# Performance work log

Measured on AMD Instinct MI355X. Metric: run time of the kernel, lower is better.

## Reference

```python
import jax, jax.numpy as jnp
import numpy as np

N = 50000      # num nodes
E = 800000     # num edges (before self loops)
H = 2          # heads
C = 64         # out_channels (== in_dim, extra_layer=False)
L = 3          # n_layer
SLOPE = 0.2    # leaky_relu negative_slope


def setup_inputs() -> dict:
    key = jax.random.key(0)
    k1, k2, k3 = jax.random.split(key, 3)
    x = jax.random.normal(k1, (N, C), dtype=jnp.float32)
    edge_index = jax.random.randint(k2, (2, E), 0, N)
    att = jax.random.normal(k3, (L, H, C), dtype=jnp.float32) * 0.1  # glorot-ish scale
    bias = jnp.zeros((L, C), dtype=jnp.float32)
    return {"x": x, "edge_index": edge_index, "att": att, "bias": bias}


def _segment_softmax(alpha, dst, n):
    # alpha: [Etot, H], softmax over edges sharing the same destination node
    m = jax.ops.segment_max(alpha, dst, num_segments=n)          # [N, H]
    a = jnp.exp(alpha - m[dst])                                  # [Etot, H]
    s = jax.ops.segment_sum(a, dst, num_segments=n)              # [N, H]
    return a / (s[dst] + 1e-16)


def _gat_layer(x, src, dst, att_l, bias_l):
    # extra_layer=False: x_l == x_r == x broadcast over heads, so x_i + x_j is
    # head-independent; compute it once as [Etot, C].
    m = jax.nn.leaky_relu(x[dst] + x[src], negative_slope=SLOPE)  # [Etot, C]
    alpha = m @ att_l.T                                           # [Etot, H]
    alpha = _segment_softmax(alpha, dst, N)
    # message = x_j * alpha, scatter-add to destinations, then mean over heads
    outs = [jax.ops.segment_sum(x[src] * alpha[:, h:h + 1], dst, num_segments=N)
            for h in range(H)]                                    # H x [N, C]
    return jnp.stack(outs, 0).mean(0) + bias_l                    # [N, C]


def reference(x, edge_index, att, bias):
    # add self loops (add_self_loops=True)
    loops = jnp.arange(N, dtype=edge_index.dtype)
    src = jnp.concatenate([edge_index[0], loops])
    dst = jnp.concatenate([edge_index[1], loops])
    feats = [x]
    h = x
    for l in range(L):
        h = _gat_layer(h, src, dst, att[l], bias[l])
        feats.append(h)
    return jnp.stack(feats, axis=1).mean(axis=1)  # [N, C]
```

## Files before the change

### kernel.cpp

```cpp
#include <hip/hip_runtime.h>
#include <hip/hip_bf16.h>

#define NN 50000
#define EE 800000
#define CC 64
#define HH 2
#define LL 3
#define CAP 64
#define NB 782
#define BCAP 1280
#define CHUNK 8192
#define NBLK ((EE + CHUNK - 1) / CHUNK)


__global__ __launch_bounds__(1024) void k_bin(const int* __restrict__ ei,
                                              int* __restrict__ bcnt,
                                              unsigned int* __restrict__ bucket) {
    __shared__ unsigned int stash[CHUNK];
    __shared__ int hist[NB];
    __shared__ int rank[NB];
    __shared__ int base[NB];

    int c0 = blockIdx.x * CHUNK;
    int n = EE - c0; if (n > CHUNK) n = CHUNK;

    for (int b = threadIdx.x; b < NB; b += 1024) { hist[b] = 0; rank[b] = 0; }
    __syncthreads();

    for (int k = threadIdx.x; k < n; k += 1024) {
        unsigned int s = (unsigned int)ei[c0 + k];
        unsigned int d = (unsigned int)ei[EE + c0 + k];
        stash[k] = (d << 16) | s;
        atomicAdd(&hist[d >> 6], 1);
    }
    __syncthreads();

    for (int b = threadIdx.x; b < NB; b += 1024) {
        int c = hist[b];
        base[b] = c ? atomicAdd(&bcnt[b], c) : 0;
    }
    __syncthreads();

    for (int k = threadIdx.x; k < n; k += 1024) {
        unsigned int pk = stash[k];
        int b = (int)(pk >> 22);
        int r = atomicAdd(&rank[b], 1);
        int pos = base[b] + r;
        if (pos < BCAP) bucket[(size_t)b * BCAP + pos] = pk;
    }
}

__global__ __launch_bounds__(256) void k_place(const unsigned int* __restrict__ bucket,
                                               const int* __restrict__ bcnt,
                                               int* __restrict__ cnt,
                                               unsigned short* __restrict__ slots) {
    __shared__ int lcnt[64];
    int b = blockIdx.x;
    if (threadIdx.x < 64) lcnt[threadIdx.x] = 0;
    __syncthreads();
    int node0 = b << 6;
    int m = bcnt[b];
    if (m > BCAP) m = BCAP;
    const unsigned int* src = bucket + (size_t)b * BCAP;
    for (int i = threadIdx.x; i < m; i += 256) {
        unsigned int pk = src[i];
        int d = (int)(pk >> 16);
        int s = (int)(pk & 0xFFFFu);
        int pos = atomicAdd(&lcnt[d - node0], 1);
        if (pos < CAP) slots[(size_t)d * CAP + pos] = (unsigned short)s;
    }
    __syncthreads();
    if (threadIdx.x < 64) {
        int node = node0 + threadIdx.x;
        if (node < NN) cnt[node] = lcnt[threadIdx.x];
    }
}


#define LEAKY(v) fmaxf((v), 0.2f * (v))

template <bool FIRST>
__global__ __launch_bounds__(256) void k_gat(const float* __restrict__ h,
                                             const int* __restrict__ cnt,
                                             const unsigned short* __restrict__ slots,
                                             const float* __restrict__ att_l,
                                             const float* __restrict__ bias_l,
                                             float* __restrict__ h_out,
                                             float* __restrict__ acc, int n) {
    int wid = threadIdx.x >> 6;
    int lane = threadIdx.x & 63;
    int node = blockIdx.x * 4 + wid;
    if (node >= n) return;
    int sub = lane >> 4, q = lane & 15;
    unsigned qb = (unsigned)q << 4;
    const char* hb = (const char*)h;
    float4 a0q = ((const float4*)att_l)[q];
    float4 a1q = ((const float4*)att_l)[16 + q];
    float4 hd = *(const float4*)(hb + (((unsigned)node << 8) + qb));
    int deg = cnt[node];
    if (deg > CAP) deg = CAP;
    const unsigned* rowu = (const unsigned*)(slots + (size_t)node * CAP);

    float s0, s1;
    float4 A0, A1;

    {
        float vx = LEAKY(2.f * hd.x), vy = LEAKY(2.f * hd.y);
        float vz = LEAKY(2.f * hd.z), vw = LEAKY(2.f * hd.w);
        float p0 = vx * a0q.x + vy * a0q.y + vz * a0q.z + vw * a0q.w;
        float p1 = vx * a1q.x + vy * a1q.y + vz * a1q.z + vw * a1q.w;
#pragma unroll
        for (int m = 8; m; m >>= 1) {
            p0 += __shfl_xor(p0, m);
            p1 += __shfl_xor(p1, m);
        }
        float e0 = 0.25f * __expf(p0), e1 = 0.25f * __expf(p1);
        s0 = e0; s1 = e1;
        A0.x = e0 * hd.x; A0.y = e0 * hd.y; A0.z = e0 * hd.z; A0.w = e0 * hd.w;
        A1.x = e1 * hd.x; A1.y = e1 * hd.y; A1.z = e1 * hd.z; A1.w = e1 * hd.w;
    }

    int npair = deg >> 1;
    for (int p = sub; p < npair; p += 4) {
        unsigned pk = rowu[p];
        float4 va = *(const float4*)(hb + (((pk & 0xFFFFu) << 8) + qb));
        float4 vb = *(const float4*)(hb + (((pk >> 16) << 8) + qb));
        float vx, vy, vz, vw;
        vx = LEAKY(va.x + hd.x); vy = LEAKY(va.y + hd.y);
        vz = LEAKY(va.z + hd.z); vw = LEAKY(va.w + hd.w);
        float pa0 = vx * a0q.x + vy * a0q.y + vz * a0q.z + vw * a0q.w;
        float pa1 = vx * a1q.x + vy * a1q.y + vz * a1q.z + vw * a1q.w;
        vx = LEAKY(vb.x + hd.x); vy = LEAKY(vb.y + hd.y);
        vz = LEAKY(vb.z + hd.z); vw = LEAKY(vb.w + hd.w);
        float pb0 = vx * a0q.x + vy * a0q.y + vz * a0q.z + vw * a0q.w;
        float pb1 = vx * a1q.x + vy * a1q.y + vz * a1q.z + vw * a1q.w;
#pragma unroll
        for (int m = 8; m; m >>= 1) {
            pa0 += __shfl_xor(pa0, m); pa1 += __shfl_xor(pa1, m);
            pb0 += __shfl_xor(pb0, m); pb1 += __shfl_xor(pb1, m);
        }
        float ea0 = __expf(pa0), ea1 = __expf(pa1);
        float eb0 = __expf(pb0), eb1 = __expf(pb1);
        s0 += ea0 + eb0;
        s1 += ea1 + eb1;
        A0.x += ea0 * va.x + eb0 * vb.x; A0.y += ea0 * va.y + eb0 * vb.y;
        A0.z += ea0 * va.z + eb0 * vb.z; A0.w += ea0 * va.w + eb0 * vb.w;
        A1.x += ea1 * va.x + eb1 * vb.x; A1.y += ea1 * va.y + eb1 * vb.y;
        A1.z += ea1 * va.z + eb1 * vb.z; A1.w += ea1 * va.w + eb1 * vb.w;
    }

    if (deg & 1) {
        int t = deg - 1;
        if (sub == ((t >> 1) & 3)) {
            unsigned s = ((const unsigned short*)rowu)[t];
            float4 hv = *(const float4*)(hb + ((s << 8) + qb));
            float vx = LEAKY(hv.x + hd.x), vy = LEAKY(hv.y + hd.y);
            float vz = LEAKY(hv.z + hd.z), vw = LEAKY(hv.w + hd.w);
            float p0 = vx * a0q.x + vy * a0q.y + vz * a0q.z + vw * a0q.w;
            float p1 = vx * a1q.x + vy * a1q.y + vz * a1q.z + vw * a1q.w;
#pragma unroll
            for (int m = 8; m; m >>= 1) {
                p0 += __shfl_xor(p0, m);
                p1 += __shfl_xor(p1, m);
            }
            float e0 = __expf(p0), e1 = __expf(p1);
            s0 += e0; s1 += e1;
            A0.x += e0 * hv.x; A0.y += e0 * hv.y; A0.z += e0 * hv.z; A0.w += e0 * hv.w;
            A1.x += e1 * hv.x; A1.y += e1 * hv.y; A1.z += e1 * hv.z; A1.w += e1 * hv.w;
        }
    }

#pragma unroll
    for (int step = 16; step <= 32; step <<= 1) {
        s0 += __shfl_xor(s0, step);
        s1 += __shfl_xor(s1, step);
        A0.x += __shfl_xor(A0.x, step); A0.y += __shfl_xor(A0.y, step);
        A0.z += __shfl_xor(A0.z, step); A0.w += __shfl_xor(A0.w, step);
        A1.x += __shfl_xor(A1.x, step); A1.y += __shfl_xor(A1.y, step);
        A1.z += __shfl_xor(A1.z, step); A1.w += __shfl_xor(A1.w, step);
    }

    if (sub == 0) {
        float inv0 = 0.5f / (s0 + 1e-16f);
        float inv1 = 0.5f / (s1 + 1e-16f);
        float4 b4 = ((const float4*)bias_l)[q];
        float4 o;
        o.x = A0.x * inv0 + A1.x * inv1 + b4.x;
        o.y = A0.y * inv0 + A1.y * inv1 + b4.y;
        o.z = A0.z * inv0 + A1.z * inv1 + b4.z;
        o.w = A0.w * inv0 + A1.w * inv1 + b4.w;
        ((float4*)h_out)[(size_t)node * 16 + q] = o;
        float4* accp = (float4*)acc + (size_t)node * 16 + q;
        float4 ac;
        if (FIRST) {
            ac.x = 0.25f * (hd.x + o.x); ac.y = 0.25f * (hd.y + o.y);
            ac.z = 0.25f * (hd.z + o.z); ac.w = 0.25f * (hd.w + o.w);
        } else {
            ac = *accp;
            ac.x += 0.25f * o.x; ac.y += 0.25f * o.y;
            ac.z += 0.25f * o.z; ac.w += 0.25f * o.w;
        }
        *accp = ac;
    }
}


static inline size_t align256(size_t x) { return (x + 255) & ~(size_t)255; }

extern "C" void kernel_launch(void* const* d_in, const int* in_sizes, int n_in,
                              void* d_out, int out_size, void* d_ws, size_t ws_size,
                              hipStream_t stream) {
    const float* x    = (const float*)d_in[0];
    const int*   ei   = (const int*)d_in[1];
    const float* att  = (const float*)d_in[2];
    const float* bias = (const float*)d_in[3];
    float* acc = (float*)d_out;

    char* w = (char*)d_ws;
    int* bcnt   = (int*)w;              w += align256((size_t)NB * sizeof(int));
    int* cnt    = (int*)w;              w += align256((size_t)NN * sizeof(int));
    unsigned int* bucket = (unsigned int*)w;
    w += align256((size_t)NB * BCAP * sizeof(unsigned int));
    unsigned short* slots = (unsigned short*)w;
    w += align256((size_t)NN * CAP * sizeof(unsigned short));
    float* hA   = (float*)w;            w += align256((size_t)NN * CC * sizeof(float));
    float* hB   = (float*)w;            w += align256((size_t)NN * CC * sizeof(float));

    const int B = 256;

    hipMemsetAsync(bcnt, 0, (size_t)NB * sizeof(int), stream);
    k_bin<<<NBLK, 1024, 0, stream>>>(ei, bcnt, bucket);
    k_place<<<NB, B, 0, stream>>>(bucket, bcnt, cnt, slots);

    k_gat<true><<<(NN + 3) / 4, B, 0, stream>>>(
        x, cnt, slots, att, bias, hA, acc, NN);
    k_gat<false><<<(NN + 3) / 4, B, 0, stream>>>(
        hA, cnt, slots, att + (size_t)HH * CC, bias + CC, hB, acc, NN);
    k_gat<false><<<(NN + 3) / 4, B, 0, stream>>>(
        hB, cnt, slots, att + (size_t)2 * HH * CC, bias + 2 * CC, hA, acc, NN);
}
```

Baseline: 218.5 us.

## Use 8-lane groups with DPP reductions in GAT aggregation kernel

Changes the per-node wave layout from 4 sub-groups of 16 lanes (float4 per lane) to 8 sub-groups of 8 lanes (two float4s per lane), so each wave handles more edge pairs concurrently. The attention dot-product reductions now use DPP row operations instead of cross-lane shuffles, and the self-loop weight is rescaled for 8 groups. The final cross-group merge is done once with DPP plus shuffles before the output write. This cuts shuffle/LDS traffic and latency per edge, at the cost of more registers per lane and more partial accumulators to merge.

```diff
diff --git a/kernel.cpp b/kernel.cpp
--- a/kernel.cpp
+++ b/kernel.cpp
@@ -78,6 +78,39 @@
 
 
 #define LEAKY(v) fmaxf((v), 0.2f * (v))
+
+template <int CTRL>
+__device__ __forceinline__ float dpp_add(float v) {
+    int t = __builtin_amdgcn_update_dpp(0, __float_as_int(v), CTRL, 0xF, 0xF, true);
+    return v + __int_as_float(t);
+}
+
+__device__ __forceinline__ float red8(float v) {
+    v = dpp_add<0xB1>(v);
+    v = dpp_add<0x4E>(v);
+    v = dpp_add<0x141>(v);
+    return v;
+}
+
+__device__ __forceinline__ float merge8(float v) {
+    v = dpp_add<0x128>(v);
+    v += __shfl_xor(v, 16);
+    v += __shfl_xor(v, 32);
+    return v;
+}
+
+__device__ __forceinline__ float4 addleaky(float4 v, float4 d) {
+    float4 r;
+    r.x = LEAKY(v.x + d.x); r.y = LEAKY(v.y + d.y);
+    r.z = LEAKY(v.z + d.z); r.w = LEAKY(v.w + d.w);
+    return r;
+}
+
+__device__ __forceinline__ float dot8(float4 al, float4 ah, float4 vl, float4 vh) {
+    float lo = fmaf(vl.w, al.w, fmaf(vl.z, al.z, fmaf(vl.y, al.y, vl.x * al.x)));
+    float hi = fmaf(vh.w, ah.w, fmaf(vh.z, ah.z, fmaf(vh.y, ah.y, vh.x * ah.x)));
+    return lo + hi;
+}
 
 template <bool FIRST>
 __global__ __launch_bounds__(256) void k_gat(const float* __restrict__ h,
@@ -91,116 +124,134 @@
     int lane = threadIdx.x & 63;
     int node = blockIdx.x * 4 + wid;
     if (node >= n) return;
-    int sub = lane >> 4, q = lane & 15;
-    unsigned qb = (unsigned)q << 4;
-    const char* hb = (const char*)h;
-    float4 a0q = ((const float4*)att_l)[q];
-    float4 a1q = ((const float4*)att_l)[16 + q];
-    float4 hd = *(const float4*)(hb + (((unsigned)node << 8) + qb));
+    int sub = lane >> 3, t = lane & 7;
+    unsigned tb = (unsigned)t << 5;
+    const char* hl = (const char*)h + tb;
+    const float4* attq = (const float4*)att_l;
+    float4 a0l = attq[2 * t],      a0h = attq[2 * t + 1];
+    float4 a1l = attq[16 + 2 * t], a1h = attq[16 + 2 * t + 1];
+    float4 hdl = *(const float4*)(hl + ((unsigned)node << 8));
+    float4 hdh = *(const float4*)(hl + ((unsigned)node << 8) + 16);
     int deg = cnt[node];
     if (deg > CAP) deg = CAP;
     const unsigned* rowu = (const unsigned*)(slots + (size_t)node * CAP);
 
     float s0, s1;
-    float4 A0, A1;
+    float4 A0l, A0h, A1l, A1h;
 
     {
-        float vx = LEAKY(2.f * hd.x), vy = LEAKY(2.f * hd.y);
-        float vz = LEAKY(2.f * hd.z), vw = LEAKY(2.f * hd.w);
-        float p0 = vx * a0q.x + vy * a0q.y + vz * a0q.z + vw * a0q.w;
-        float p1 = vx * a1q.x + vy * a1q.y + vz * a1q.z + vw * a1q.w;
-#pragma unroll
-        for (int m = 8; m; m >>= 1) {
-            p0 += __shfl_xor(p0, m);
-            p1 += __shfl_xor(p1, m);
-        }
-        float e0 = 0.25f * __expf(p0), e1 = 0.25f * __expf(p1);
+        float4 u = addleaky(hdl, hdl);
+        float4 v = addleaky(hdh, hdh);
+        float p0 = red8(dot8(a0l, a0h, u, v));
+        float p1 = red8(dot8(a1l, a1h, u, v));
+        float e0 = 0.125f * __expf(p0), e1 = 0.125f * __expf(p1);
         s0 = e0; s1 = e1;
-        A0.x = e0 * hd.x; A0.y = e0 * hd.y; A0.z = e0 * hd.z; A0.w = e0 * hd.w;
-        A1.x = e1 * hd.x; A1.y = e1 * hd.y; A1.z = e1 * hd.z; A1.w = e1 * hd.w;
+        A0l.x = e0 * hdl.x; A0l.y = e0 * hdl.y; A0l.z = e0 * hdl.z; A0l.w = e0 * hdl.w;
+        A0h.x = e0 * hdh.x; A0h.y = e0 * hdh.y; A0h.z = e0 * hdh.z; A0h.w = e0 * hdh.w;
+        A1l.x = e1 * hdl.x; A1l.y = e1 * hdl.y; A1l.z = e1 * hdl.z; A1l.w = e1 * hdl.w;
+        A1h.x = e1 * hdh.x; A1h.y = e1 * hdh.y; A1h.z = e1 * hdh.z; A1h.w = e1 * hdh.w;
     }
 
     int npair = deg >> 1;
-    for (int p = sub; p < npair; p += 4) {
+    for (int p = sub; p < npair; p += 8) {
         unsigned pk = rowu[p];
-        float4 va = *(const float4*)(hb + (((pk & 0xFFFFu) << 8) + qb));
-        float4 vb = *(const float4*)(hb + (((pk >> 16) << 8) + qb));
-        float vx, vy, vz, vw;
-        vx = LEAKY(va.x + hd.x); vy = LEAKY(va.y + hd.y);
-        vz = LEAKY(va.z + hd.z); vw = LEAKY(va.w + hd.w);
-        float pa0 = vx * a0q.x + vy * a0q.y + vz * a0q.z + vw * a0q.w;
-        float pa1 = vx * a1q.x + vy * a1q.y + vz * a1q.z + vw * a1q.w;
-        vx = LEAKY(vb.x + hd.x); vy = LEAKY(vb.y + hd.y);
-        vz = LEAKY(vb.z + hd.z); vw = LEAKY(vb.w + hd.w);
-        float pb0 = vx * a0q.x + vy * a0q.y + vz * a0q.z + vw * a0q.w;
-        float pb1 = vx * a1q.x + vy * a1q.y + vz * a1q.z + vw * a1q.w;
-#pragma unroll
-        for (int m = 8; m; m >>= 1) {
-            pa0 += __shfl_xor(pa0, m); pa1 += __shfl_xor(pa1, m);
-            pb0 += __shfl_xor(pb0, m); pb1 += __shfl_xor(pb1, m);
-        }
+        unsigned oa = (pk & 0xFFFFu) << 8;
+        unsigned ob = (pk & 0xFFFF0000u) >> 8;
+        float4 va_l = *(const float4*)(hl + oa);
+        float4 va_h = *(const float4*)(hl + oa + 16);
+        float4 vb_l = *(const float4*)(hl + ob);
+        float4 vb_h = *(const float4*)(hl + ob + 16);
+        float4 la_l = addleaky(va_l, hdl), la_h = addleaky(va_h, hdh);
+        float4 lb_l = addleaky(vb_l, hdl), lb_h = addleaky(vb_h, hdh);
+        float pa0 = red8(dot8(a0l, a0h, la_l, la_h));
+        float pa1 = red8(dot8(a1l, a1h, la_l, la_h));
+        float pb0 = red8(dot8(a0l, a0h, lb_l, lb_h));
+        float pb1 = red8(dot8(a1l, a1h, lb_l, lb_h));
         float ea0 = __expf(pa0), ea1 = __expf(pa1);
         float eb0 = __expf(pb0), eb1 = __expf(pb1);
         s0 += ea0 + eb0;
         s1 += ea1 + eb1;
-        A0.x += ea0 * va.x + eb0 * vb.x; A0.y += ea0 * va.y + eb0 * vb.y;
-        A0.z += ea0 * va.z + eb0 * vb.z; A0.w += ea0 * va.w + eb0 * vb.w;
-        A1.x += ea1 * va.x + eb1 * vb.x; A1.y += ea1 * va.y + eb1 * vb.y;
-        A1.z += ea1 * va.z + eb1 * vb.z; A1.w += ea1 * va.w + eb1 * vb.w;
+        A0l.x = fmaf(ea0, va_l.x, fmaf(eb0, vb_l.x, A0l.x));
+        A0l.y = fmaf(ea0, va_l.y, fmaf(eb0, vb_l.y, A0l.y));
+        A0l.z = fmaf(ea0, va_l.z, fmaf(eb0, vb_l.z, A0l.z));
+        A0l.w = fmaf(ea0, va_l.w, fmaf(eb0, vb_l.w, A0l.w));
+        A0h.x = fmaf(ea0, va_h.x, fmaf(eb0, vb_h.x, A0h.x));
+        A0h.y = fmaf(ea0, va_h.y, fmaf(eb0, vb_h.y, A0h.y));
+        A0h.z = fmaf(ea0, va_h.z, fmaf(eb0, vb_h.z, A0h.z));
+        A0h.w = fmaf(ea0, va_h.w, fmaf(eb0, vb_h.w, A0h.w));
+        A1l.x = fmaf(ea1, va_l.x, fmaf(eb1, vb_l.x, A1l.x));
+        A1l.y = fmaf(ea1, va_l.y, fmaf(eb1, vb_l.y, A1l.y));
+        A1l.z = fmaf(ea1, va_l.z, fmaf(eb1, vb_l.z, A1l.z));
+        A1l.w = fmaf(ea1, va_l.w, fmaf(eb1, vb_l.w, A1l.w));
+        A1h.x = fmaf(ea1, va_h.x, fmaf(eb1, vb_h.x, A1h.x));
+        A1h.y = fmaf(ea1, va_h.y, fmaf(eb1, vb_h.y, A1h.y));
+        A1h.z = fmaf(ea1, va_h.z, fmaf(eb1, vb_h.z, A1h.z));
+        A1h.w = fmaf(ea1, va_h.w, fmaf(eb1, vb_h.w, A1h.w));
     }
 
     if (deg & 1) {
-        int t = deg - 1;
-        if (sub == ((t >> 1) & 3)) {
-            unsigned s = ((const unsigned short*)rowu)[t];
-            float4 hv = *(const float4*)(hb + ((s << 8) + qb));
-            float vx = LEAKY(hv.x + hd.x), vy = LEAKY(hv.y + hd.y);
-            float vz = LEAKY(hv.z + hd.z), vw = LEAKY(hv.w + hd.w);
-            float p0 = vx * a0q.x + vy * a0q.y + vz * a0q.z + vw * a0q.w;
-            float p1 = vx * a1q.x + vy * a1q.y + vz * a1q.z + vw * a1q.w;
-#pragma unroll
-            for (int m = 8; m; m >>= 1) {
-                p0 += __shfl_xor(p0, m);
-                p1 += __shfl_xor(p1, m);
-            }
+        int tl = deg - 1;
+        if (sub == (npair & 7)) {
+            unsigned s = ((const unsigned short*)rowu)[tl];
+            unsigned o = s << 8;
+            float4 v_l = *(const float4*)(hl + o);
+            float4 v_h = *(const float4*)(hl + o + 16);
+            float4 l_l = addleaky(v_l, hdl), l_h = addleaky(v_h, hdh);
+            float p0 = red8(dot8(a0l, a0h, l_l, l_h));
+            float p1 = red8(dot8(a1l, a1h, l_l, l_h));
             float e0 = __expf(p0), e1 = __expf(p1);
             s0 += e0; s1 += e1;
-            A0.x += e0 * hv.x; A0.y += e0 * hv.y; A0.z += e0 * hv.z; A0.w += e0 * hv.w;
-            A1.x += e1 * hv.x; A1.y += e1 * hv.y; A1.z += e1 * hv.z; A1.w += e1 * hv.w;
+            A0l.x = fmaf(e0, v_l.x, A0l.x); A0l.y = fmaf(e0, v_l.y, A0l.y);
+            A0l.z = fmaf(e0, v_l.z, A0l.z); A0l.w = fmaf(e0, v_l.w, A0l.w);
+            A0h.x = fmaf(e0, v_h.x, A0h.x); A0h.y = fmaf(e0, v_h.y, A0h.y);
+            A0h.z = fmaf(e0, v_h.z, A0h.z); A0h.w = fmaf(e0, v_h.w, A0h.w);
+            A1l.x = fmaf(e1, v_l.x, A1l.x); A1l.y = fmaf(e1, v_l.y, A1l.y);
+            A1l.z = fmaf(e1, v_l.z, A1l.z); A1l.w = fmaf(e1, v_l.w, A1l.w);
+            A1h.x = fmaf(e1, v_h.x, A1h.x); A1h.y = fmaf(e1, v_h.y, A1h.y);
+            A1h.z = fmaf(e1, v_h.z, A1h.z); A1h.w = fmaf(e1, v_h.w, A1h.w);
         }
     }
 
-#pragma unroll
-    for (int step = 16; step <= 32; step <<= 1) {
-        s0 += __shfl_xor(s0, step);
-        s1 += __shfl_xor(s1, step);
-        A0.x += __shfl_xor(A0.x, step); A0.y += __shfl_xor(A0.y, step);
-        A0.z += __shfl_xor(A0.z, step); A0.w += __shfl_xor(A0.w, step);
-        A1.x += __shfl_xor(A1.x, step); A1.y += __shfl_xor(A1.y, step);
-        A1.z += __shfl_xor(A1.z, step); A1.w += __shfl_xor(A1.w, step);
-    }
+    s0 = merge8(s0);
+    s1 = merge8(s1);
+    float inv0 = 0.5f / (s0 + 1e-16f);
+    float inv1 = 0.5f / (s1 + 1e-16f);
+    float4 o_l, o_h;
+    o_l.x = fmaf(A1l.x, inv1, A0l.x * inv0);
+    o_l.y = fmaf(A1l.y, inv1, A0l.y * inv0);
+    o_l.z = fmaf(A1l.z, inv1, A0l.z * inv0);
+    o_l.w = fmaf(A1l.w, inv1, A0l.w * inv0);
+    o_h.x = fmaf(A1h.x, inv1, A0h.x * inv0);
+    o_h.y = fmaf(A1h.y, inv1, A0h.y * inv0);
+    o_h.z = fmaf(A1h.z, inv1, A0h.z * inv0);
+    o_h.w = fmaf(A1h.w, inv1, A0h.w * inv0);
+    o_l.x = merge8(o_l.x); o_l.y = merge8(o_l.y);
+    o_l.z = merge8(o_l.z); o_l.w = merge8(o_l.w);
+    o_h.x = merge8(o_h.x); o_h.y = merge8(o_h.y);
+    o_h.z = merge8(o_h.z); o_h.w = merge8(o_h.w);
 
     if (sub == 0) {
-        float inv0 = 0.5f / (s0 + 1e-16f);
-        float inv1 = 0.5f / (s1 + 1e-16f);
-        float4 b4 = ((const float4*)bias_l)[q];
-        float4 o;
-        o.x = A0.x * inv0 + A1.x * inv1 + b4.x;
-        o.y = A0.y * inv0 + A1.y * inv1 + b4.y;
-        o.z = A0.z * inv0 + A1.z * inv1 + b4.z;
-        o.w = A0.w * inv0 + A1.w * inv1 + b4.w;
-        ((float4*)h_out)[(size_t)node * 16 + q] = o;
-        float4* accp = (float4*)acc + (size_t)node * 16 + q;
-        float4 ac;
+        float4 b_l = ((const float4*)bias_l)[2 * t];
+        float4 b_h = ((const float4*)bias_l)[2 * t + 1];
+        o_l.x += b_l.x; o_l.y += b_l.y; o_l.z += b_l.z; o_l.w += b_l.w;
+        o_h.x += b_h.x; o_h.y += b_h.y; o_h.z += b_h.z; o_h.w += b_h.w;
+        float4* outp = (float4*)h_out + (size_t)node * 16 + 2 * t;
+        outp[0] = o_l; outp[1] = o_h;
+        float4* accp = (float4*)acc + (size_t)node * 16 + 2 * t;
+        float4 c0, c1;
         if (FIRST) {
-            ac.x = 0.25f * (hd.x + o.x); ac.y = 0.25f * (hd.y + o.y);
-            ac.z = 0.25f * (hd.z + o.z); ac.w = 0.25f * (hd.w + o.w);
+            c0.x = 0.25f * (hdl.x + o_l.x); c0.y = 0.25f * (hdl.y + o_l.y);
+            c0.z = 0.25f * (hdl.z + o_l.z); c0.w = 0.25f * (hdl.w + o_l.w);
+            c1.x = 0.25f * (hdh.x + o_h.x); c1.y = 0.25f * (hdh.y + o_h.y);
+            c1.z = 0.25f * (hdh.z + o_h.z); c1.w = 0.25f * (hdh.w + o_h.w);
         } else {
-            ac = *accp;
-            ac.x += 0.25f * o.x; ac.y += 0.25f * o.y;
-            ac.z += 0.25f * o.z; ac.w += 0.25f * o.w;
+            c0 = accp[0]; c1 = accp[1];
+            c0.x += 0.25f * o_l.x; c0.y += 0.25f * o_l.y;
+            c0.z += 0.25f * o_l.z; c0.w += 0.25f * o_l.w;
+            c1.x += 0.25f * o_h.x; c1.y += 0.25f * o_h.y;
+            c1.z += 0.25f * o_h.z; c1.w += 0.25f * o_h.w;
         }
-        *accp = ac;
+        accp[0] = c0; accp[1] = c1;
     }
 }
 
```

Measured after the change: 236.0 us. +8.0%, slower.
